# Performance work log

Measured on AMD Instinct MI355X. Metric: run time of the kernel, lower is better.

Reference implementation:

```python
import jax, jax.numpy as jnp
import numpy as np

DIM = 2048
HID = 2730  # dim*mlp_ratio // (1 + top_k)
E = 8
K = 2
B, T = 4, 2048


def setup_inputs() -> dict:
    key = jax.random.key(0)
    ks = jax.random.split(key, 8)
    s = 0.02
    return {
        "x": jax.random.normal(ks[0], (B, T, DIM), jnp.float32),
        "router_w": jax.random.normal(ks[1], (DIM, E), jnp.float32) * s,
        "sw1": jax.random.normal(ks[2], (DIM, HID), jnp.float32) * s,
        "sw2": jax.random.normal(ks[3], (HID, DIM), jnp.float32) * s,
        "sw3": jax.random.normal(ks[4], (DIM, HID), jnp.float32) * s,
        "ew1": jax.random.normal(ks[5], (E, DIM, HID), jnp.float32) * s,
        "ew2": jax.random.normal(ks[6], (E, HID, DIM), jnp.float32) * s,
        "ew3": jax.random.normal(ks[7], (E, DIM, HID), jnp.float32) * s,
    }


def _expert(x, w1, w2, w3):
    return (jax.nn.silu(x @ w1) * (x @ w3)) @ w2


def reference(x, router_w, sw1, sw2, sw3, ew1, ew2, ew3):
    # eval-mode forward (no router noise, no aux loss)
    out = _expert(x, sw1, sw2, sw3)  # shared expert, [B,T,C]
    logits = x @ router_w            # [B,T,E]
    probs = jax.nn.softmax(logits, axis=-1)
    topv, topi = jax.lax.top_k(probs, K)           # [B,T,K]
    topv = topv / topv.sum(-1, keepdims=True)      # renormalize
    # dense combine weights [B,T,E]: w[...,e] = sum_k topv_k * (topi_k == e)
    onehot = jax.nn.one_hot(topi, E, dtype=x.dtype)  # [B,T,K,E]
    w = jnp.einsum("btk,btke->bte", topv, onehot)
    for e in range(E):  # fixed small loop over experts
        out = out + w[..., e:e + 1] * _expert(x, ew1[e], ew2[e], ew3[e])
    return out
```

## Files before the change

### kernel.cpp

```cpp
#include <hip/hip_runtime.h>
#include <hip/hip_bf16.h>
#include <stdio.h>

#define DIM 2048
#define HID 2730
#define HID_PAD 2816
#define NE 8
#define NTOK 8192
#define NROWS 24576

typedef __bf16 v8bf __attribute__((ext_vector_type(8)));
typedef float v4f  __attribute__((ext_vector_type(4)));

__device__ __forceinline__ void gload16(const void* g, void* l){
  __builtin_amdgcn_global_load_lds((const __attribute__((address_space(1))) void*)g,
                                   (__attribute__((address_space(3))) void*)l, 16, 0, 0);
}


__global__ void moe_zero_i(int* __restrict__ p, int n){
  int i = threadIdx.x;
  if (i < n) p[i] = 0;
}

__global__ void moe_cast_x(const float* __restrict__ x, __hip_bfloat16* __restrict__ xb){
  int i = (blockIdx.x*blockDim.x + threadIdx.x)*4;
  float4 v = *reinterpret_cast<const float4*>(x + i);
  __hip_bfloat16 o[4];
  o[0]=__float2bfloat16(v.x); o[1]=__float2bfloat16(v.y);
  o[2]=__float2bfloat16(v.z); o[3]=__float2bfloat16(v.w);
  unsigned long long u; __builtin_memcpy(&u, o, 8);
  *reinterpret_cast<unsigned long long*>(xb + i) = u;
}

__global__ void moe_tcast(const float* __restrict__ srcE, const float* __restrict__ srcS,
                          __hip_bfloat16* __restrict__ dst, int R, int C, int Cp, int Rp){
  int e = blockIdx.z;
  const float* src = (e < NE) ? (srcE + (size_t)e*R*C) : srcS;
  __hip_bfloat16* d = dst + (size_t)e*Cp*Rp;
  __shared__ float tile[32][33];
  int c0 = blockIdx.x*32, r0 = blockIdx.y*32;
  #pragma unroll
  for (int i=0;i<4;i++){
    int r = r0 + threadIdx.y + i*8, c = c0 + threadIdx.x;
    float v = (r < R && c < C) ? src[(size_t)r*C + c] : 0.0f;
    tile[threadIdx.y + i*8][threadIdx.x] = v;
  }
  __syncthreads();
  #pragma unroll
  for (int i=0;i<4;i++){
    int c = c0 + threadIdx.y + i*8, r = r0 + threadIdx.x;
    if (c < Cp && r < Rp)
      d[(size_t)c*Rp + r] = __float2bfloat16(tile[threadIdx.x][threadIdx.y + i*8]);
  }
}


__global__ __launch_bounds__(256) void moe_router(
    const float* __restrict__ x, const float* __restrict__ rw,
    float* __restrict__ topw, int* __restrict__ cnt, int* __restrict__ bucket){
  int wav = threadIdx.x >> 6, lane = threadIdx.x & 63;
  int t = blockIdx.x*4 + wav;
  const float* xr = x + (size_t)t*DIM;
  float a[NE];
  #pragma unroll
  for (int e=0;e<NE;e++) a[e]=0.f;
  for (int d0 = lane; d0 < DIM; d0 += 64){
    float xv = xr[d0];
    const float* rr = rw + d0*NE;
    #pragma unroll
    for (int e=0;e<NE;e++) a[e] += xv * rr[e];
  }
  #pragma unroll
  for (int e=0;e<NE;e++){
    float v = a[e];
    #pragma unroll
    for (int o=32;o>0;o>>=1) v += __shfl_xor(v, o);
    a[e]=v;
  }
  if (lane == 0){
    float m = a[0];
    for (int e=1;e<NE;e++) m = fmaxf(m, a[e]);
    float p[NE];
    for (int e=0;e<NE;e++) p[e] = expf(a[e]-m);
    int e0=0;
    for (int e=1;e<NE;e++) if (p[e] > p[e0]) e0=e;
    int e1 = (e0==0)?1:0;
    for (int e=0;e<NE;e++) if (e!=e0 && p[e] > p[e1]) e1=e;
    float ss = p[e0]+p[e1];
    topw[t*2]   = p[e0]/ss;
    topw[t*2+1] = p[e1]/ss;
    int p0 = atomicAdd(&cnt[e0],1); bucket[e0*16384 + p0] = t*2;
    int p1 = atomicAdd(&cnt[e1],1); bucket[e1*16384 + p1] = t*2+1;
  }
}

__global__ void moe_prefix(const int* __restrict__ cnt, int* __restrict__ base){
  if (threadIdx.x==0 && blockIdx.x==0){
    int b=0; base[0]=0;
    for (int e=0;e<NE;e++){ b += cnt[e]; base[e+1]=b; }
    base[9] = base[8] + NTOK;
  }
}

__global__ void moe_fill(const int* __restrict__ cnt, const int* __restrict__ base,
                         const int* __restrict__ bucket, const float* __restrict__ topw,
                         int* __restrict__ row_token, float* __restrict__ row_weight,
                         int* __restrict__ inv){
  int idx = blockIdx.x*blockDim.x + threadIdx.x;
  if (idx < NE*16384){
    int e = idx >> 14, p = idx & 16383;
    if (p < cnt[e]){
      int slot = bucket[idx];
      int row = base[e] + p;
      row_token[row]  = slot >> 1;
      row_weight[row] = topw[slot];
      inv[slot] = row;
    }
  } else {
    int t = idx - NE*16384;
    row_token[16384 + t]  = t;
    row_weight[16384 + t] = 1.0f;
  }
}


#define BM1 256
#define BN1 128
#define NT1 64

__global__ __launch_bounds__(512, 2) void moe_gemm1(
    const __hip_bfloat16* __restrict__ xb,
    const __hip_bfloat16* __restrict__ w1t,
    const __hip_bfloat16* __restrict__ w3t,
    const int* __restrict__ row_token,
    const int* __restrict__ base_,
    __hip_bfloat16* __restrict__ g)
{
  int e = blockIdx.z;
  int base = base_[e];
  int cnt  = base_[e+1] - base;
  int m0 = blockIdx.y * BM1;
  if (m0 >= cnt) return;
  int xp = (blockIdx.x & 7)*3 + (blockIdx.x >> 3);
  if (xp >= 22) return;
  int n0 = xp * BN1;

  __shared__ __align__(16) unsigned short lA [4][BM1][32];
  __shared__ __align__(16) unsigned short lB1[4][BN1][32];
  __shared__ __align__(16) unsigned short lB3[4][BN1][32];
  __shared__ int tok[BM1];

  int tid = threadIdx.x;
  if (tid < BM1){
    int r = m0 + tid;
    tok[tid] = row_token[base + (r < cnt ? r : m0)];
  }
  __syncthreads();

  const __hip_bfloat16* w1e = w1t + (size_t)e*HID_PAD*DIM;
  const __hip_bfloat16* w3e = w3t + (size_t)e*HID_PAD*DIM;

  int wav = tid >> 6, lane = tid & 63;

  int c0 = tid,        r0c = c0 >> 2;
  int q0 = ((c0 & 3) ^ ((r0c >> 1) & 3)) * 8;
  int c1 = tid + 512,  r1c = c1 >> 2;
  int q1 = ((c1 & 3) ^ ((r1c >> 1) & 3)) * 8;
  const __hip_bfloat16* aS0 = xb  + (size_t)tok[r0c]*DIM + q0;
  const __hip_bfloat16* aS1 = xb  + (size_t)tok[r1c]*DIM + q1;
  const __hip_bfloat16* b1S = w1e + (size_t)(n0 + r0c)*DIM + q0;
  const __hip_bfloat16* b3S = w3e + (size_t)(n0 + r0c)*DIM + q0;

  int wm = (wav >> 2) * 128;
  int wn = (wav & 3) * 32;
  int lm = lane & 15, lq = lane >> 4;
  int sl = ((lq ^ ((lm >> 1) & 3)) << 3);

  v4f acc1[8][2], acc3[8][2];
  v4f vz = {0.f,0.f,0.f,0.f};
  #pragma unroll
  for (int i=0;i<8;i++)
    #pragma unroll
    for (int j=0;j<2;j++){ acc1[i][j]=vz; acc3[i][j]=vz; }

  #pragma unroll
  for (int tt=0; tt<3; ++tt){
    int kk = tt*32;
    gload16(aS0 + kk, &lA [tt][0][0] + wav*512);
    gload16(aS1 + kk, &lA [tt][0][0] + wav*512 + 4096);
    gload16(b1S + kk, &lB1[tt][0][0] + wav*512);
    gload16(b3S + kk, &lB3[tt][0][0] + wav*512);
  }

  for (int t = 0; t < NT1; ++t){
    if (t < NT1-2)       asm volatile("s_waitcnt vmcnt(8)" ::: "memory");
    else if (t == NT1-2) asm volatile("s_waitcnt vmcnt(4)" ::: "memory");
    else                 asm volatile("s_waitcnt vmcnt(0)" ::: "memory");
    __builtin_amdgcn_s_barrier();
    asm volatile("" ::: "memory");

    int b = t & 3;
    v8bf b1f[2], b3f[2], af[4];
    #pragma unroll
    for (int j=0;j<2;j++){
      b1f[j] = *reinterpret_cast<const v8bf*>(&lB1[b][wn + j*16 + lm][sl]);
      b3f[j] = *reinterpret_cast<const v8bf*>(&lB3[b][wn + j*16 + lm][sl]);
    }
    #pragma unroll
    for (int i=0;i<4;i++)
      af[i] = *reinterpret_cast<const v8bf*>(&lA[b][wm + i*16 + lm][sl]);

    if (t + 3 < NT1){
      int kk = (t+3)*32, nb = (t+3) & 3;
      gload16(aS0 + kk, &lA [nb][0][0] + wav*512);
      gload16(aS1 + kk, &lA [nb][0][0] + wav*512 + 4096);
      gload16(b1S + kk, &lB1[nb][0][0] + wav*512);
      gload16(b3S + kk, &lB3[nb][0][0] + wav*512);
    }

    __builtin_amdgcn_s_setprio(1);
    #pragma unroll
    for (int i=0;i<4;i++)
      #pragma unroll
      for (int j=0;j<2;j++){
        acc1[i][j] = __builtin_amdgcn_mfma_f32_16x16x32_bf16(af[i], b1f[j], acc1[i][j], 0,0,0);
        acc3[i][j] = __builtin_amdgcn_mfma_f32_16x16x32_bf16(af[i], b3f[j], acc3[i][j], 0,0,0);
      }
    __builtin_amdgcn_s_setprio(0);

    #pragma unroll
    for (int i=0;i<4;i++)
      af[i] = *reinterpret_cast<const v8bf*>(&lA[b][wm + 64 + i*16 + lm][sl]);

    __builtin_amdgcn_s_setprio(1);
    #pragma unroll
    for (int i=0;i<4;i++)
      #pragma unroll
      for (int j=0;j<2;j++){
        acc1[4+i][j] = __builtin_amdgcn_mfma_f32_16x16x32_bf16(af[i], b1f[j], acc1[4+i][j], 0,0,0);
        acc3[4+i][j] = __builtin_amdgcn_mfma_f32_16x16x32_bf16(af[i], b3f[j], acc3[4+i][j], 0,0,0);
      }
    __builtin_amdgcn_s_setprio(0);
  }

  #pragma unroll
  for (int i=0;i<8;i++){
    #pragma unroll
    for (int r=0;r<4;r++){
      int ml = wm + i*16 + lq*4 + r;
      if (m0 + ml < cnt){
        size_t grow = (size_t)(base + m0 + ml) * HID_PAD;
        #pragma unroll
        for (int j=0;j<2;j++){
          float s1 = acc1[i][j][r];
          float s3 = acc3[i][j][r];
          float gv = (s1 / (1.0f + __expf(-s1))) * s3;
          g[grow + n0 + wn + j*16 + lm] = __float2bfloat16(gv);
        }
      }
    }
  }
}


#define BM2 256
#define BN2 256
#define NT2 88

__global__ __launch_bounds__(512, 2) void moe_gemm2(
    const __hip_bfloat16* __restrict__ g,
    const __hip_bfloat16* __restrict__ w2t,
    const float* __restrict__ row_weight,
    const int* __restrict__ base_,
    float* __restrict__ y)
{
  int e = blockIdx.z;
  int base = base_[e];
  int cnt  = base_[e+1] - base;
  int m0 = blockIdx.y * BM2;
  if (m0 >= cnt) return;
  int n0 = blockIdx.x * BN2;

  __shared__ __align__(16) unsigned short lA[4][BM2][32];
  __shared__ __align__(16) unsigned short lB[4][BN2][32];
  __shared__ float wgt[BM2];

  int tid = threadIdx.x;
  if (tid < BM2){
    int r = m0 + tid;
    wgt[tid] = (r < cnt) ? row_weight[base + r] : 0.0f;
  }
  __syncthreads();

  const __hip_bfloat16* w2e = w2t + (size_t)e*DIM*HID_PAD;
  int wav = tid >> 6, lane = tid & 63;

  int c0 = tid,        r0c = c0 >> 2;
  int q0 = ((c0 & 3) ^ ((r0c >> 1) & 3)) * 8;
  int c1 = tid + 512,  r1c = c1 >> 2;
  int q1 = ((c1 & 3) ^ ((r1c >> 1) & 3)) * 8;
  const __hip_bfloat16* aS0 = g   + (size_t)(base + m0 + r0c)*HID_PAD + q0;
  const __hip_bfloat16* aS1 = g   + (size_t)(base + m0 + r1c)*HID_PAD + q1;
  const __hip_bfloat16* bS0 = w2e + (size_t)(n0 + r0c)*HID_PAD + q0;
  const __hip_bfloat16* bS1 = w2e + (size_t)(n0 + r1c)*HID_PAD + q1;

  int wm = (wav >> 2) * 128;
  int wn = (wav & 3) * 64;
  int lm = lane & 15, lq = lane >> 4;
  int sl = ((lq ^ ((lm >> 1) & 3)) << 3);

  v4f acc[8][4];
  v4f vz = {0.f,0.f,0.f,0.f};
  #pragma unroll
  for (int i=0;i<8;i++)
    #pragma unroll
    for (int j=0;j<4;j++) acc[i][j]=vz;

  #pragma unroll
  for (int tt=0; tt<3; ++tt){
    int kk = tt*32;
    gload16(aS0 + kk, &lA[tt][0][0] + wav*512);
    gload16(aS1 + kk, &lA[tt][0][0] + wav*512 + 4096);
    gload16(bS0 + kk, &lB[tt][0][0] + wav*512);
    gload16(bS1 + kk, &lB[tt][0][0] + wav*512 + 4096);
  }

  for (int t = 0; t < NT2; ++t){
    if (t < NT2-2)       asm volatile("s_waitcnt vmcnt(8)" ::: "memory");
    else if (t == NT2-2) asm volatile("s_waitcnt vmcnt(4)" ::: "memory");
    else                 asm volatile("s_waitcnt vmcnt(0)" ::: "memory");
    __builtin_amdgcn_s_barrier();
    asm volatile("" ::: "memory");

    int b = t & 3;
    v8bf bf4[4], af[4];
    #pragma unroll
    for (int j=0;j<4;j++)
      bf4[j] = *reinterpret_cast<const v8bf*>(&lB[b][wn + j*16 + lm][sl]);
    #pragma unroll
    for (int i=0;i<4;i++)
      af[i] = *reinterpret_cast<const v8bf*>(&lA[b][wm + i*16 + lm][sl]);

    if (t + 3 < NT2){
      int kk = (t+3)*32, nb = (t+3) & 3;
      gload16(aS0 + kk, &lA[nb][0][0] + wav*512);
      gload16(aS1 + kk, &lA[nb][0][0] + wav*512 + 4096);
      gload16(bS0 + kk, &lB[nb][0][0] + wav*512);
      gload16(bS1 + kk, &lB[nb][0][0] + wav*512 + 4096);
    }

    __builtin_amdgcn_s_setprio(1);
    #pragma unroll
    for (int i=0;i<4;i++)
      #pragma unroll
      for (int j=0;j<4;j++)
        acc[i][j] = __builtin_amdgcn_mfma_f32_16x16x32_bf16(af[i], bf4[j], acc[i][j], 0,0,0);
    __builtin_amdgcn_s_setprio(0);

    #pragma unroll
    for (int i=0;i<4;i++)
      af[i] = *reinterpret_cast<const v8bf*>(&lA[b][wm + 64 + i*16 + lm][sl]);

    __builtin_amdgcn_s_setprio(1);
    #pragma unroll
    for (int i=0;i<4;i++)
      #pragma unroll
      for (int j=0;j<4;j++)
        acc[4+i][j] = __builtin_amdgcn_mfma_f32_16x16x32_bf16(af[i], bf4[j], acc[4+i][j], 0,0,0);
    __builtin_amdgcn_s_setprio(0);
  }

  #pragma unroll
  for (int i=0;i<8;i++){
    #pragma unroll
    for (int r=0;r<4;r++){
      int ml = wm + i*16 + lq*4 + r;
      if (m0 + ml < cnt){
        float wv = wgt[ml];
        size_t yrow = (size_t)(base + m0 + ml) * DIM;
        #pragma unroll
        for (int j=0;j<4;j++)
          y[yrow + n0 + wn + j*16 + lm] = wv * acc[i][j][r];
      }
    }
  }
}


__global__ __launch_bounds__(256) void moe_combine(
    const float4* __restrict__ y, const int* __restrict__ inv, float4* __restrict__ out){
  int idx = blockIdx.x*blockDim.x + threadIdx.x;
  int t = idx >> 9, d = idx & 511;
  float4 s = y[(((size_t)16384 + t) << 9) + d];
  int r0 = inv[t*2], r1 = inv[t*2+1];
  float4 a = y[((size_t)r0 << 9) + d];
  float4 b = y[((size_t)r1 << 9) + d];
  s.x += a.x + b.x; s.y += a.y + b.y; s.z += a.z + b.z; s.w += a.w + b.w;
  out[idx] = s;
}


extern "C" void kernel_launch(void* const* d_in, const int* in_sizes, int n_in,
                              void* d_out, int out_size, void* d_ws, size_t ws_size,
                              hipStream_t stream) {
  const float* x   = (const float*)d_in[0];
  const float* rw  = (const float*)d_in[1];
  const float* sw1 = (const float*)d_in[2];
  const float* sw2 = (const float*)d_in[3];
  const float* sw3 = (const float*)d_in[4];
  const float* ew1 = (const float*)d_in[5];
  const float* ew2 = (const float*)d_in[6];
  const float* ew3 = (const float*)d_in[7];
  float* out = (float*)d_out;

  char* ws = (char*)d_ws;
  size_t off = 0;
  auto nxt = [&](size_t b) -> char* {
    char* p = ws + off; off += (b + 255) & ~(size_t)255; return p;
  };
  __hip_bfloat16* xb  = (__hip_bfloat16*)nxt((size_t)NTOK*DIM*2);
  __hip_bfloat16* w1t = (__hip_bfloat16*)nxt((size_t)9*HID_PAD*DIM*2);
  __hip_bfloat16* w3t = (__hip_bfloat16*)nxt((size_t)9*HID_PAD*DIM*2);
  __hip_bfloat16* w2t = (__hip_bfloat16*)nxt((size_t)9*DIM*HID_PAD*2);
  __hip_bfloat16* g   = (__hip_bfloat16*)nxt((size_t)NROWS*HID_PAD*2);
  float* topw      = (float*)nxt(16384*4);
  int*   cnt       = (int*)  nxt(32);
  int*   base_     = (int*)  nxt(64);
  int*   bucket    = (int*)  nxt(NE*16384*4);
  int*   row_token = (int*)  nxt(NROWS*4);
  float* row_weight= (float*)nxt(NROWS*4);
  int*   inv       = (int*)  nxt(16384*4);

  static_assert((size_t)NROWS*DIM*4 <= 2*((size_t)9*HID_PAD*DIM*2), "y alias overflow");
  float* y = (float*)w1t;

  if (off > ws_size) {
    fprintf(stderr, "MoE kernel: ws too small (%zu needed, %zu given)\n", off, ws_size);
    return;
  }

  moe_zero_i<<<1, 32, 0, stream>>>(cnt, NE);
  moe_cast_x<<<16384, 256, 0, stream>>>(x, xb);

  dim3 tb(32,8);
  moe_tcast<<<dim3(88,64,9), tb, 0, stream>>>(ew1, sw1, w1t, DIM, HID, HID_PAD, DIM);
  moe_tcast<<<dim3(88,64,9), tb, 0, stream>>>(ew3, sw3, w3t, DIM, HID, HID_PAD, DIM);
  moe_tcast<<<dim3(64,88,9), tb, 0, stream>>>(ew2, sw2, w2t, HID, DIM, DIM, HID_PAD);

  moe_router<<<NTOK/4, 256, 0, stream>>>(x, rw, topw, cnt, bucket);
  moe_prefix<<<1, 1, 0, stream>>>(cnt, base_);
  moe_fill<<<544, 256, 0, stream>>>(cnt, base_, bucket, topw, row_token, row_weight, inv);

  moe_gemm1<<<dim3(24,32,9), 512, 0, stream>>>(xb, w1t, w3t, row_token, base_, g);
  moe_gemm2<<<dim3(8,32,9), 512, 0, stream>>>(g, w2t, row_weight, base_, y);
  moe_combine<<<16384, 256, 0, stream>>>((const float4*)y, inv, (float4*)out);
}
```

Before: 2.018 ms.

## Restructure MoE GEMMs into K=64 double-buffered ping-pong pipeline with interleaved staging

Both expert GEMMs move from a 4-stage K=32 LDS ring to a 2-stage K=64 double buffer with an 8-way XOR swizzle. Each iteration is split into four MFMA quadrants, with the next tile's global-to-LDS loads spread between them and barriers placed around each phase, so memory traffic is issued alongside compute. The gemm1 grid drops the block remapping and the idle padded blocks. The extra barriers per iteration and the shallower prefetch depth may add stalls.

```diff
diff --git a/kernel.cpp b/kernel.cpp
--- a/kernel.cpp
+++ b/kernel.cpp
@@ -127,7 +127,7 @@
 
 #define BM1 256
 #define BN1 128
-#define NT1 64
+#define NT1 32
 
 __global__ __launch_bounds__(512, 2) void moe_gemm1(
     const __hip_bfloat16* __restrict__ xb,
@@ -142,13 +142,11 @@
   int cnt  = base_[e+1] - base;
   int m0 = blockIdx.y * BM1;
   if (m0 >= cnt) return;
-  int xp = (blockIdx.x & 7)*3 + (blockIdx.x >> 3);
-  if (xp >= 22) return;
-  int n0 = xp * BN1;
-
-  __shared__ __align__(16) unsigned short lA [4][BM1][32];
-  __shared__ __align__(16) unsigned short lB1[4][BN1][32];
-  __shared__ __align__(16) unsigned short lB3[4][BN1][32];
+  int n0 = blockIdx.x * BN1;
+
+  __shared__ __align__(16) unsigned short lA [2][BM1][64];
+  __shared__ __align__(16) unsigned short lB1[2][BN1][64];
+  __shared__ __align__(16) unsigned short lB3[2][BN1][64];
   __shared__ int tok[BM1];
 
   int tid = threadIdx.x;
@@ -163,19 +161,38 @@
 
   int wav = tid >> 6, lane = tid & 63;
 
-  int c0 = tid,        r0c = c0 >> 2;
-  int q0 = ((c0 & 3) ^ ((r0c >> 1) & 3)) * 8;
-  int c1 = tid + 512,  r1c = c1 >> 2;
-  int q1 = ((c1 & 3) ^ ((r1c >> 1) & 3)) * 8;
-  const __hip_bfloat16* aS0 = xb  + (size_t)tok[r0c]*DIM + q0;
-  const __hip_bfloat16* aS1 = xb  + (size_t)tok[r1c]*DIM + q1;
-  const __hip_bfloat16* b1S = w1e + (size_t)(n0 + r0c)*DIM + q0;
-  const __hip_bfloat16* b3S = w3e + (size_t)(n0 + r0c)*DIM + q0;
-
-  int wm = (wav >> 2) * 128;
-  int wn = (wav & 3) * 32;
+  int rr = (wav*64 + lane) >> 3;
+  int qq = (((wav*64 + lane) & 7) ^ (rr & 7)) * 8;
+
+  const __hip_bfloat16* aP0 = xb + (size_t)tok[rr      ]*DIM + qq;
+  const __hip_bfloat16* aP1 = xb + (size_t)tok[rr +  64]*DIM + qq;
+  const __hip_bfloat16* aP2 = xb + (size_t)tok[rr + 128]*DIM + qq;
+  const __hip_bfloat16* aP3 = xb + (size_t)tok[rr + 192]*DIM + qq;
+  const __hip_bfloat16* b1P0 = w1e + (size_t)(n0 + rr     )*DIM + qq;
+  const __hip_bfloat16* b1P1 = w1e + (size_t)(n0 + rr + 64)*DIM + qq;
+  const __hip_bfloat16* b3P0 = w3e + (size_t)(n0 + rr     )*DIM + qq;
+  const __hip_bfloat16* b3P1 = w3e + (size_t)(n0 + rr + 64)*DIM + qq;
+
+  int lbase0 = (wav*64)*8, lbase1 = (512 + wav*64)*8;
+
+  auto stageAlo = [&](int t){ int kk = t*64, d = t&1;
+    gload16(aP0 + kk, &lA[d][0][0] + lbase0);
+    gload16(aP1 + kk, &lA[d][0][0] + lbase1); };
+  auto stageAhi = [&](int t){ int kk = t*64, d = t&1;
+    gload16(aP2 + kk, &lA[d][128][0] + lbase0);
+    gload16(aP3 + kk, &lA[d][128][0] + lbase1); };
+  auto stageB1 = [&](int t){ int kk = t*64, d = t&1;
+    gload16(b1P0 + kk, &lB1[d][0][0] + lbase0);
+    gload16(b1P1 + kk, &lB1[d][0][0] + lbase1); };
+  auto stageB3 = [&](int t){ int kk = t*64, d = t&1;
+    gload16(b3P0 + kk, &lB3[d][0][0] + lbase0);
+    gload16(b3P1 + kk, &lB3[d][0][0] + lbase1); };
+
+  int wm = wav >> 2, wn = wav & 3;
   int lm = lane & 15, lq = lane >> 4;
-  int sl = ((lq ^ ((lm >> 1) & 3)) << 3);
+  int sk = lm & 7;
+  int eo0 = ((    lq) ^ sk) * 8;
+  int eo1 = ((4 + lq) ^ sk) * 8;
 
   v4f acc1[8][2], acc3[8][2];
   v4f vz = {0.f,0.f,0.f,0.f};
@@ -184,71 +201,99 @@
     #pragma unroll
     for (int j=0;j<2;j++){ acc1[i][j]=vz; acc3[i][j]=vz; }
 
-  #pragma unroll
-  for (int tt=0; tt<3; ++tt){
-    int kk = tt*32;
-    gload16(aS0 + kk, &lA [tt][0][0] + wav*512);
-    gload16(aS1 + kk, &lA [tt][0][0] + wav*512 + 4096);
-    gload16(b1S + kk, &lB1[tt][0][0] + wav*512);
-    gload16(b3S + kk, &lB3[tt][0][0] + wav*512);
-  }
+  stageAlo(0); stageAhi(0); stageB1(0); stageB3(0);
+  stageAlo(1); stageAhi(1);
+  asm volatile("s_waitcnt vmcnt(4)" ::: "memory");
+  __builtin_amdgcn_s_barrier();
 
   for (int t = 0; t < NT1; ++t){
-    if (t < NT1-2)       asm volatile("s_waitcnt vmcnt(8)" ::: "memory");
-    else if (t == NT1-2) asm volatile("s_waitcnt vmcnt(4)" ::: "memory");
-    else                 asm volatile("s_waitcnt vmcnt(0)" ::: "memory");
-    __builtin_amdgcn_s_barrier();
-    asm volatile("" ::: "memory");
-
-    int b = t & 3;
-    v8bf b1f[2], b3f[2], af[4];
+    int d = t & 1;
+    v8bf a0k0[4], a0k1[4], b1k0[2], b1k1[2];
+    #pragma unroll
+    for (int i=0;i<4;i++){
+      a0k0[i] = *reinterpret_cast<const v8bf*>(&lA[d][wm*128 + i*16 + lm][eo0]);
+      a0k1[i] = *reinterpret_cast<const v8bf*>(&lA[d][wm*128 + i*16 + lm][eo1]);
+    }
     #pragma unroll
     for (int j=0;j<2;j++){
-      b1f[j] = *reinterpret_cast<const v8bf*>(&lB1[b][wn + j*16 + lm][sl]);
-      b3f[j] = *reinterpret_cast<const v8bf*>(&lB3[b][wn + j*16 + lm][sl]);
-    }
-    #pragma unroll
-    for (int i=0;i<4;i++)
-      af[i] = *reinterpret_cast<const v8bf*>(&lA[b][wm + i*16 + lm][sl]);
-
-    if (t + 3 < NT1){
-      int kk = (t+3)*32, nb = (t+3) & 3;
-      gload16(aS0 + kk, &lA [nb][0][0] + wav*512);
-      gload16(aS1 + kk, &lA [nb][0][0] + wav*512 + 4096);
-      gload16(b1S + kk, &lB1[nb][0][0] + wav*512);
-      gload16(b3S + kk, &lB3[nb][0][0] + wav*512);
-    }
-
-    __builtin_amdgcn_s_setprio(1);
-    #pragma unroll
-    for (int i=0;i<4;i++)
-      #pragma unroll
-      for (int j=0;j<2;j++){
-        acc1[i][j] = __builtin_amdgcn_mfma_f32_16x16x32_bf16(af[i], b1f[j], acc1[i][j], 0,0,0);
-        acc3[i][j] = __builtin_amdgcn_mfma_f32_16x16x32_bf16(af[i], b3f[j], acc3[i][j], 0,0,0);
-      }
-    __builtin_amdgcn_s_setprio(0);
-
-    #pragma unroll
-    for (int i=0;i<4;i++)
-      af[i] = *reinterpret_cast<const v8bf*>(&lA[b][wm + 64 + i*16 + lm][sl]);
-
-    __builtin_amdgcn_s_setprio(1);
-    #pragma unroll
-    for (int i=0;i<4;i++)
-      #pragma unroll
-      for (int j=0;j<2;j++){
-        acc1[4+i][j] = __builtin_amdgcn_mfma_f32_16x16x32_bf16(af[i], b1f[j], acc1[4+i][j], 0,0,0);
-        acc3[4+i][j] = __builtin_amdgcn_mfma_f32_16x16x32_bf16(af[i], b3f[j], acc3[4+i][j], 0,0,0);
-      }
-    __builtin_amdgcn_s_setprio(0);
+      b1k0[j] = *reinterpret_cast<const v8bf*>(&lB1[d][wn*32 + j*16 + lm][eo0]);
+      b1k1[j] = *reinterpret_cast<const v8bf*>(&lB1[d][wn*32 + j*16 + lm][eo1]);
+    }
+    if (t+1 < NT1) stageB1(t+1);
+    __builtin_amdgcn_s_barrier();
+    asm volatile("s_waitcnt lgkmcnt(0)" ::: "memory");
+    __builtin_amdgcn_s_setprio(1);
+    #pragma unroll
+    for (int i=0;i<4;i++)
+      #pragma unroll
+      for (int j=0;j<2;j++){
+        acc1[i][j] = __builtin_amdgcn_mfma_f32_16x16x32_bf16(a0k0[i], b1k0[j], acc1[i][j], 0,0,0);
+        acc1[i][j] = __builtin_amdgcn_mfma_f32_16x16x32_bf16(a0k1[i], b1k1[j], acc1[i][j], 0,0,0);
+      }
+    __builtin_amdgcn_s_setprio(0);
+    __builtin_amdgcn_s_barrier();
+
+    v8bf a1k0[4], a1k1[4];
+    #pragma unroll
+    for (int i=0;i<4;i++){
+      a1k0[i] = *reinterpret_cast<const v8bf*>(&lA[d][wm*128 + 64 + i*16 + lm][eo0]);
+      a1k1[i] = *reinterpret_cast<const v8bf*>(&lA[d][wm*128 + 64 + i*16 + lm][eo1]);
+    }
+    if (t+1 < NT1) stageB3(t+1);
+    __builtin_amdgcn_s_barrier();
+    asm volatile("s_waitcnt lgkmcnt(0)" ::: "memory");
+    __builtin_amdgcn_s_setprio(1);
+    #pragma unroll
+    for (int i=0;i<4;i++)
+      #pragma unroll
+      for (int j=0;j<2;j++){
+        acc1[4+i][j] = __builtin_amdgcn_mfma_f32_16x16x32_bf16(a1k0[i], b1k0[j], acc1[4+i][j], 0,0,0);
+        acc1[4+i][j] = __builtin_amdgcn_mfma_f32_16x16x32_bf16(a1k1[i], b1k1[j], acc1[4+i][j], 0,0,0);
+      }
+    __builtin_amdgcn_s_setprio(0);
+    __builtin_amdgcn_s_barrier();
+
+    v8bf b3k0[2], b3k1[2];
+    #pragma unroll
+    for (int j=0;j<2;j++){
+      b3k0[j] = *reinterpret_cast<const v8bf*>(&lB3[d][wn*32 + j*16 + lm][eo0]);
+      b3k1[j] = *reinterpret_cast<const v8bf*>(&lB3[d][wn*32 + j*16 + lm][eo1]);
+    }
+    if (t+2 < NT1) stageAlo(t+2);
+    __builtin_amdgcn_s_barrier();
+    asm volatile("s_waitcnt lgkmcnt(0)" ::: "memory");
+    __builtin_amdgcn_s_setprio(1);
+    #pragma unroll
+    for (int i=0;i<4;i++)
+      #pragma unroll
+      for (int j=0;j<2;j++){
+        acc3[4+i][j] = __builtin_amdgcn_mfma_f32_16x16x32_bf16(a1k0[i], b3k0[j], acc3[4+i][j], 0,0,0);
+        acc3[4+i][j] = __builtin_amdgcn_mfma_f32_16x16x32_bf16(a1k1[i], b3k1[j], acc3[4+i][j], 0,0,0);
+      }
+    __builtin_amdgcn_s_setprio(0);
+    __builtin_amdgcn_s_barrier();
+
+    if (t+2 < NT1) stageAhi(t+2);
+    __builtin_amdgcn_s_barrier();
+    __builtin_amdgcn_s_setprio(1);
+    #pragma unroll
+    for (int i=0;i<4;i++)
+      #pragma unroll
+      for (int j=0;j<2;j++){
+        acc3[i][j] = __builtin_amdgcn_mfma_f32_16x16x32_bf16(a0k0[i], b3k0[j], acc3[i][j], 0,0,0);
+        acc3[i][j] = __builtin_amdgcn_mfma_f32_16x16x32_bf16(a0k1[i], b3k1[j], acc3[i][j], 0,0,0);
+      }
+    __builtin_amdgcn_s_setprio(0);
+    if (t+2 < NT1) asm volatile("s_waitcnt vmcnt(4)" ::: "memory");
+    else           asm volatile("s_waitcnt vmcnt(0)" ::: "memory");
+    __builtin_amdgcn_s_barrier();
   }
 
   #pragma unroll
   for (int i=0;i<8;i++){
     #pragma unroll
     for (int r=0;r<4;r++){
-      int ml = wm + i*16 + lq*4 + r;
+      int ml = wm*128 + i*16 + lq*4 + r;
       if (m0 + ml < cnt){
         size_t grow = (size_t)(base + m0 + ml) * HID_PAD;
         #pragma unroll
@@ -256,7 +301,7 @@
           float s1 = acc1[i][j][r];
           float s3 = acc3[i][j][r];
           float gv = (s1 / (1.0f + __expf(-s1))) * s3;
-          g[grow + n0 + wn + j*16 + lm] = __float2bfloat16(gv);
+          g[grow + n0 + wn*32 + j*16 + lm] = __float2bfloat16(gv);
         }
       }
     }
@@ -266,7 +311,7 @@
 
 #define BM2 256
 #define BN2 256
-#define NT2 88
+#define NT2 44
 
 __global__ __launch_bounds__(512, 2) void moe_gemm2(
     const __hip_bfloat16* __restrict__ g,
@@ -282,8 +327,8 @@
   if (m0 >= cnt) return;
   int n0 = blockIdx.x * BN2;
 
-  __shared__ __align__(16) unsigned short lA[4][BM2][32];
-  __shared__ __align__(16) unsigned short lB[4][BN2][32];
+  __shared__ __align__(16) unsigned short lA[2][BM2][64];
+  __shared__ __align__(16) unsigned short lB[2][BN2][64];
   __shared__ float wgt[BM2];
 
   int tid = threadIdx.x;
@@ -296,19 +341,38 @@
   const __hip_bfloat16* w2e = w2t + (size_t)e*DIM*HID_PAD;
   int wav = tid >> 6, lane = tid & 63;
 
-  int c0 = tid,        r0c = c0 >> 2;
-  int q0 = ((c0 & 3) ^ ((r0c >> 1) & 3)) * 8;
-  int c1 = tid + 512,  r1c = c1 >> 2;
-  int q1 = ((c1 & 3) ^ ((r1c >> 1) & 3)) * 8;
-  const __hip_bfloat16* aS0 = g   + (size_t)(base + m0 + r0c)*HID_PAD + q0;
-  const __hip_bfloat16* aS1 = g   + (size_t)(base + m0 + r1c)*HID_PAD + q1;
-  const __hip_bfloat16* bS0 = w2e + (size_t)(n0 + r0c)*HID_PAD + q0;
-  const __hip_bfloat16* bS1 = w2e + (size_t)(n0 + r1c)*HID_PAD + q1;
-
-  int wm = (wav >> 2) * 128;
-  int wn = (wav & 3) * 64;
+  int rr = (wav*64 + lane) >> 3;
+  int qq = (((wav*64 + lane) & 7) ^ (rr & 7)) * 8;
+
+  const __hip_bfloat16* aP0 = g + (size_t)(base + m0 + rr      )*HID_PAD + qq;
+  const __hip_bfloat16* aP1 = g + (size_t)(base + m0 + rr +  64)*HID_PAD + qq;
+  const __hip_bfloat16* aP2 = g + (size_t)(base + m0 + rr + 128)*HID_PAD + qq;
+  const __hip_bfloat16* aP3 = g + (size_t)(base + m0 + rr + 192)*HID_PAD + qq;
+  const __hip_bfloat16* bP0 = w2e + (size_t)(n0 + rr      )*HID_PAD + qq;
+  const __hip_bfloat16* bP1 = w2e + (size_t)(n0 + rr +  64)*HID_PAD + qq;
+  const __hip_bfloat16* bP2 = w2e + (size_t)(n0 + rr + 128)*HID_PAD + qq;
+  const __hip_bfloat16* bP3 = w2e + (size_t)(n0 + rr + 192)*HID_PAD + qq;
+
+  int lbase0 = (wav*64)*8, lbase1 = (512 + wav*64)*8;
+
+  auto stageAlo = [&](int t){ int kk = t*64, d = t&1;
+    gload16(aP0 + kk, &lA[d][0][0] + lbase0);
+    gload16(aP1 + kk, &lA[d][0][0] + lbase1); };
+  auto stageAhi = [&](int t){ int kk = t*64, d = t&1;
+    gload16(aP2 + kk, &lA[d][128][0] + lbase0);
+    gload16(aP3 + kk, &lA[d][128][0] + lbase1); };
+  auto stageBlo = [&](int t){ int kk = t*64, d = t&1;
+    gload16(bP0 + kk, &lB[d][0][0] + lbase0);
+    gload16(bP1 + kk, &lB[d][0][0] + lbase1); };
+  auto stageBhi = [&](int t){ int kk = t*64, d = t&1;
+    gload16(bP2 + kk, &lB[d][128][0] + lbase0);
+    gload16(bP3 + kk, &lB[d][128][0] + lbase1); };
+
+  int wm = wav >> 2, wn = wav & 3;
   int lm = lane & 15, lq = lane >> 4;
-  int sl = ((lq ^ ((lm >> 1) & 3)) << 3);
+  int sk = lm & 7;
+  int eo0 = ((    lq) ^ sk) * 8;
+  int eo1 = ((4 + lq) ^ sk) * 8;
 
   v4f acc[8][4];
   v4f vz = {0.f,0.f,0.f,0.f};
@@ -317,71 +381,105 @@
     #pragma unroll
     for (int j=0;j<4;j++) acc[i][j]=vz;
 
-  #pragma unroll
-  for (int tt=0; tt<3; ++tt){
-    int kk = tt*32;
-    gload16(aS0 + kk, &lA[tt][0][0] + wav*512);
-    gload16(aS1 + kk, &lA[tt][0][0] + wav*512 + 4096);
-    gload16(bS0 + kk, &lB[tt][0][0] + wav*512);
-    gload16(bS1 + kk, &lB[tt][0][0] + wav*512 + 4096);
-  }
+  stageAlo(0); stageAhi(0); stageBlo(0); stageBhi(0);
+  stageAlo(1); stageAhi(1);
+  asm volatile("s_waitcnt vmcnt(4)" ::: "memory");
+  __builtin_amdgcn_s_barrier();
 
   for (int t = 0; t < NT2; ++t){
-    if (t < NT2-2)       asm volatile("s_waitcnt vmcnt(8)" ::: "memory");
-    else if (t == NT2-2) asm volatile("s_waitcnt vmcnt(4)" ::: "memory");
-    else                 asm volatile("s_waitcnt vmcnt(0)" ::: "memory");
-    __builtin_amdgcn_s_barrier();
-    asm volatile("" ::: "memory");
-
-    int b = t & 3;
-    v8bf bf4[4], af[4];
-    #pragma unroll
-    for (int j=0;j<4;j++)
-      bf4[j] = *reinterpret_cast<const v8bf*>(&lB[b][wn + j*16 + lm][sl]);
-    #pragma unroll
-    for (int i=0;i<4;i++)
-      af[i] = *reinterpret_cast<const v8bf*>(&lA[b][wm + i*16 + lm][sl]);
-
-    if (t + 3 < NT2){
-      int kk = (t+3)*32, nb = (t+3) & 3;
-      gload16(aS0 + kk, &lA[nb][0][0] + wav*512);
-      gload16(aS1 + kk, &lA[nb][0][0] + wav*512 + 4096);
-      gload16(bS0 + kk, &lB[nb][0][0] + wav*512);
-      gload16(bS1 + kk, &lB[nb][0][0] + wav*512 + 4096);
-    }
-
-    __builtin_amdgcn_s_setprio(1);
-    #pragma unroll
-    for (int i=0;i<4;i++)
-      #pragma unroll
-      for (int j=0;j<4;j++)
-        acc[i][j] = __builtin_amdgcn_mfma_f32_16x16x32_bf16(af[i], bf4[j], acc[i][j], 0,0,0);
-    __builtin_amdgcn_s_setprio(0);
-
-    #pragma unroll
-    for (int i=0;i<4;i++)
-      af[i] = *reinterpret_cast<const v8bf*>(&lA[b][wm + 64 + i*16 + lm][sl]);
-
-    __builtin_amdgcn_s_setprio(1);
-    #pragma unroll
-    for (int i=0;i<4;i++)
-      #pragma unroll
-      for (int j=0;j<4;j++)
-        acc[4+i][j] = __builtin_amdgcn_mfma_f32_16x16x32_bf16(af[i], bf4[j], acc[4+i][j], 0,0,0);
-    __builtin_amdgcn_s_setprio(0);
+    int d = t & 1;
+    v8bf a0k0[4], a0k1[4], bAk0[2], bAk1[2];
+    #pragma unroll
+    for (int i=0;i<4;i++){
+      a0k0[i] = *reinterpret_cast<const v8bf*>(&lA[d][wm*128 + i*16 + lm][eo0]);
+      a0k1[i] = *reinterpret_cast<const v8bf*>(&lA[d][wm*128 + i*16 + lm][eo1]);
+    }
+    #pragma unroll
+    for (int j=0;j<2;j++){
+      bAk0[j] = *reinterpret_cast<const v8bf*>(&lB[d][wn*64 + j*16 + lm][eo0]);
+      bAk1[j] = *reinterpret_cast<const v8bf*>(&lB[d][wn*64 + j*16 + lm][eo1]);
+    }
+    if (t+1 < NT2) stageBlo(t+1);
+    __builtin_amdgcn_s_barrier();
+    asm volatile("s_waitcnt lgkmcnt(0)" ::: "memory");
+    __builtin_amdgcn_s_setprio(1);
+    #pragma unroll
+    for (int i=0;i<4;i++)
+      #pragma unroll
+      for (int j=0;j<2;j++){
+        acc[i][j] = __builtin_amdgcn_mfma_f32_16x16x32_bf16(a0k0[i], bAk0[j], acc[i][j], 0,0,0);
+        acc[i][j] = __builtin_amdgcn_mfma_f32_16x16x32_bf16(a0k1[i], bAk1[j], acc[i][j], 0,0,0);
+      }
+    __builtin_amdgcn_s_setprio(0);
+    __builtin_amdgcn_s_barrier();
+
+    v8bf a1k0[4], a1k1[4];
+    #pragma unroll
+    for (int i=0;i<4;i++){
+      a1k0[i] = *reinterpret_cast<const v8bf*>(&lA[d][wm*128 + 64 + i*16 + lm][eo0]);
+      a1k1[i] = *reinterpret_cast<const v8bf*>(&lA[d][wm*128 + 64 + i*16 + lm][eo1]);
+    }
+    if (t+1 < NT2) stageBhi(t+1);
+    __builtin_amdgcn_s_barrier();
+    asm volatile("s_waitcnt lgkmcnt(0)" ::: "memory");
+    __builtin_amdgcn_s_setprio(1);
+    #pragma unroll
+    for (int i=0;i<4;i++)
+      #pragma unroll
+      for (int j=0;j<2;j++){
+        acc[4+i][j] = __builtin_amdgcn_mfma_f32_16x16x32_bf16(a1k0[i], bAk0[j], acc[4+i][j], 0,0,0);
+        acc[4+i][j] = __builtin_amdgcn_mfma_f32_16x16x32_bf16(a1k1[i], bAk1[j], acc[4+i][j], 0,0,0);
+      }
+    __builtin_amdgcn_s_setprio(0);
+    __builtin_amdgcn_s_barrier();
+
+    v8bf bBk0[2], bBk1[2];
+    #pragma unroll
+    for (int j=0;j<2;j++){
+      bBk0[j] = *reinterpret_cast<const v8bf*>(&lB[d][wn*64 + 32 + j*16 + lm][eo0]);
+      bBk1[j] = *reinterpret_cast<const v8bf*>(&lB[d][wn*64 + 32 + j*16 + lm][eo1]);
+    }
+    if (t+2 < NT2) stageAlo(t+2);
+    __builtin_amdgcn_s_barrier();
+    asm volatile("s_waitcnt lgkmcnt(0)" ::: "memory");
+    __builtin_amdgcn_s_setprio(1);
+    #pragma unroll
+    for (int i=0;i<4;i++)
+      #pragma unroll
+      for (int j=0;j<2;j++){
+        acc[4+i][2+j] = __builtin_amdgcn_mfma_f32_16x16x32_bf16(a1k0[i], bBk0[j], acc[4+i][2+j], 0,0,0);
+        acc[4+i][2+j] = __builtin_amdgcn_mfma_f32_16x16x32_bf16(a1k1[i], bBk1[j], acc[4+i][2+j], 0,0,0);
+      }
+    __builtin_amdgcn_s_setprio(0);
+    __builtin_amdgcn_s_barrier();
+
+    if (t+2 < NT2) stageAhi(t+2);
+    __builtin_amdgcn_s_barrier();
+    __builtin_amdgcn_s_setprio(1);
+    #pragma unroll
+    for (int i=0;i<4;i++)
+      #pragma unroll
+      for (int j=0;j<2;j++){
+        acc[i][2+j] = __builtin_amdgcn_mfma_f32_16x16x32_bf16(a0k0[i], bBk0[j], acc[i][2+j], 0,0,0);
+        acc[i][2+j] = __builtin_amdgcn_mfma_f32_16x16x32_bf16(a0k1[i], bBk1[j], acc[i][2+j], 0,0,0);
+      }
+    __builtin_amdgcn_s_setprio(0);
+    if (t+2 < NT2) asm volatile("s_waitcnt vmcnt(4)" ::: "memory");
+    else           asm volatile("s_waitcnt vmcnt(0)" ::: "memory");
+    __builtin_amdgcn_s_barrier();
   }
 
   #pragma unroll
   for (int i=0;i<8;i++){
     #pragma unroll
     for (int r=0;r<4;r++){
-      int ml = wm + i*16 + lq*4 + r;
+      int ml = wm*128 + i*16 + lq*4 + r;
       if (m0 + ml < cnt){
         float wv = wgt[ml];
         size_t yrow = (size_t)(base + m0 + ml) * DIM;
         #pragma unroll
         for (int j=0;j<4;j++)
-          y[yrow + n0 + wn + j*16 + lm] = wv * acc[i][j][r];
+          y[yrow + n0 + wn*64 + j*16 + lm] = wv * acc[i][j][r];
       }
     }
   }
@@ -452,7 +550,7 @@
   moe_prefix<<<1, 1, 0, stream>>>(cnt, base_);
   moe_fill<<<544, 256, 0, stream>>>(cnt, base_, bucket, topw, row_token, row_weight, inv);
 
-  moe_gemm1<<<dim3(24,32,9), 512, 0, stream>>>(xb, w1t, w3t, row_token, base_, g);
+  moe_gemm1<<<dim3(22,32,9), 512, 0, stream>>>(xb, w1t, w3t, row_token, base_, g);
   moe_gemm2<<<dim3(8,32,9), 512, 0, stream>>>(g, w2t, row_weight, base_, y);
   moe_combine<<<16384, 256, 0, stream>>>((const float4*)y, inv, (float4*)out);
 }
```

After: 2.092 ms. +3.7%, slower.
